# Kernel tuning notes

Hardware: AMD Instinct MI355X
Metric: run time of the kernel (lower is better)

Reference implementation:

```python
import jax, jax.numpy as jnp
import numpy as np

B, IN_LEN, NN, IN_DIM = 32, 28, 2048, 1
E, ND = 256, 256          # embed_dim, node_dim
H = E + ND                # hidden_dim = 512
N_LAYERS = 3
OUT_LEN = 28


def setup_inputs() -> dict:
    key = jax.random.key(0)
    ks = jax.random.split(key, 16)
    x_node = jax.random.normal(ks[0], (B, IN_LEN, NN, IN_DIM), jnp.float32)
    # x_state channels: [0]=cumulative cases, [1]=infected I, [2]=population N
    col0 = jax.random.uniform(ks[1], (B, IN_LEN, NN, 1), jnp.float32) * 100.0
    colI = jax.random.uniform(ks[2], (B, IN_LEN, NN, 1), jnp.float32) * 100.0 + 1.0
    colN = 1e4 * (1.0 + 0.1 * jax.random.uniform(ks[3], (B, IN_LEN, NN, 1), jnp.float32))
    x_state = jnp.concatenate([col0, colI, colN], axis=-1)
    node_emb = jax.random.normal(ks[4], (NN, ND), jnp.float32) * 0.05
    W_ts = jax.random.normal(ks[5], (E, IN_DIM * IN_LEN), jnp.float32) * 0.05
    b_ts = jnp.zeros((E,), jnp.float32)
    enc_W1 = jax.random.normal(ks[6], (N_LAYERS, H, H), jnp.float32) * 0.02
    enc_b1 = jnp.zeros((N_LAYERS, H), jnp.float32)
    enc_W2 = jax.random.normal(ks[7], (N_LAYERS, H, H), jnp.float32) * 0.02
    enc_b2 = jnp.zeros((N_LAYERS, H), jnp.float32)
    Wb = jax.random.normal(ks[8], (1, H), jnp.float32) * 0.05
    bb = jnp.zeros((1,), jnp.float32)
    Wg = jax.random.normal(ks[9], (1, H), jnp.float32) * 0.05
    bg = jnp.zeros((1,), jnp.float32)
    return dict(x_node=x_node, x_state=x_state, node_emb=node_emb,
                W_ts=W_ts, b_ts=b_ts, enc_W1=enc_W1, enc_b1=enc_b1,
                enc_W2=enc_W2, enc_b2=enc_b2, Wb=Wb, bb=bb, Wg=Wg, bg=bg)


def _forward(x_node, x_state, node_emb, W_ts, b_ts,
             enc_W1, enc_b1, enc_W2, enc_b2, Wb, bb, Wg, bg):
    Bn, Lh, Nn, _ = x_node.shape
    # [B,L,N,D] -> [B,N,L*D] (channel = in_dim*in_len for 1x1 conv == linear)
    flat = jnp.transpose(x_node[..., :IN_DIM], (0, 2, 1, 3)).reshape(Bn, Nn, Lh * IN_DIM)
    ts = flat @ W_ts.T + b_ts                                  # [B,N,E]
    h = jnp.concatenate(
        [ts, jnp.broadcast_to(node_emb[None], (Bn,) + node_emb.shape)], axis=-1)  # [B,N,H]
    for l in range(enc_W1.shape[0]):                            # residual MLP encoder
        z = jnp.maximum(h @ enc_W1[l].T + enc_b1[l], 0.0)
        h = h + z @ enc_W2[l].T + enc_b2[l]
    b = jax.nn.sigmoid(h @ Wb.T + bb)                           # [B,N,1] infection rate
    g = jax.nn.sigmoid(h @ Wg.T + bg)                           # [B,N,1] recovery rate

    Npop = x_state[:, -1, :, 2:3]                               # [B,N,1]
    I_hist = x_state[..., 1:2] / g[:, None]                     # [B,L,N,1]
    Iin_hist = jnp.maximum(
        I_hist[:, 1:] - I_hist[:, :-1] + x_state[:, :-1, :, 1:2], 0.0)  # [B,L-1,N,1]
    t1 = jnp.arange(Lh - 1, 0, -1, dtype=jnp.float32)
    w1 = jnp.exp(-g[:, None] * t1[None, :, None, None])         # [B,L-1,N,1]
    I_Tm1 = jnp.sum(w1 * Iin_hist, axis=1)                      # [B,N,1]
    R_Tm1 = Npop - x_state[:, -2, :, 0:1]
    S_Tm1 = Npop - I_Tm1 - R_Tm1
    Iin0 = b * S_Tm1 * I_Tm1 / Npop
    Rin0 = g * I_hist[:, -1, :, 0:1]
    Iin_hist = jnp.concatenate([Iin_hist, Iin0[:, None]], axis=1)  # [B,L,N,1]
    S = S_Tm1 - Iin0
    t2 = jnp.arange(Lh, 0, -1, dtype=jnp.float32)
    w2 = jnp.exp(-g[:, None] * t2[None, :, None, None])
    I = jnp.sum(w2 * Iin_hist, axis=1)                          # [B,N,1]
    R = R_Tm1 + Rin0

    # The torch loop recomputes sum_i exp(-g*(L-i))*Iin_i each step; exact identity:
    # I_new = exp(-g) * (I_old + Iin_new). O(T) scan instead of O(T^2).
    decay = jnp.exp(-g)

    def step(carry, _):
        S, I, R = carry
        Iin = b * S * I / Npop
        S = S - Iin
        Rin = g * I            # uses pre-update I_T, matching torch order
        I = decay * (I + Iin)
        R = R + Rin
        return (S, I, R), Rin

    _, rins = jax.lax.scan(step, (S, I, R), None, length=OUT_LEN)  # [T,B,N,1]
    return jnp.transpose(rins, (1, 0, 2, 3))                       # [B,out_len,N,1]


def reference(x_node, x_state, node_emb, W_ts, b_ts, enc_W1, enc_b1,
              enc_W2, enc_b2, Wb, bb, Wg, bg):
    return _forward(x_node, x_state, node_emb, W_ts, b_ts,
                    enc_W1, enc_b1, enc_W2, enc_b2, Wb, bb, Wg, bg)
```

## Files before the change

### kernel.cpp

```cpp
#include <hip/hip_runtime.h>
#include <hip/hip_bf16.h>
#include <math.h>

#define BATCH 32
#define IN_LEN 28
#define NN 2048
#define E 256
#define H 512
#define N_LAYERS 3
#define OUT_LEN 28
#define M_ROWS (BATCH * NN)

typedef unsigned short u16;
typedef unsigned int   u32;
typedef __attribute__((ext_vector_type(8))) short short8;
typedef __attribute__((ext_vector_type(4))) float f32x4;

#define WAITV(N)  asm volatile("s_waitcnt vmcnt(" #N ")" ::: "memory")
#define BARRIER() __builtin_amdgcn_s_barrier()

__device__ __forceinline__ u16 f2h(float x) {
    union { _Float16 h; u16 u; } v; v.h = (_Float16)x; return v.u;
}
__device__ __forceinline__ float h2f(u16 u) {
    union { _Float16 h; u16 u; } v; v.u = u; return (float)v.h;
}

__device__ __forceinline__ void gload_lds16(const void* g, void* l) {
    __builtin_amdgcn_global_load_lds(
        (const __attribute__((address_space(1))) void*)g,
        (__attribute__((address_space(3))) void*)l, 16, 0, 0);
}

__global__ __launch_bounds__(256)
void k_split2(const float* __restrict__ w1, const float* __restrict__ w2,
              u16* __restrict__ hi, u16* __restrict__ lo, int nW)
{
    int i = blockIdx.x * 256 + threadIdx.x;
    float v = (i < nW) ? w1[i] : w2[i - nW];
    u16 h = f2h(v);
    hi[i] = h;
    lo[i] = f2h(v - h2f(h));
}

__global__ __launch_bounds__(256)
void k_ts(const float* __restrict__ x_node, const float* __restrict__ node_emb,
          const float* __restrict__ W_ts, const float* __restrict__ b_ts,
          u16* __restrict__ hhi, u16* __restrict__ hlo)
{
    __shared__ float xs[IN_LEN][64];
    const int tid = threadIdx.x;
    const int b   = blockIdx.y;
    const int n0  = blockIdx.x * 64;
    const int c   = tid & 127;
    const int sec = tid >> 7;

    for (int idx = tid; idx < IN_LEN * 64; idx += 256) {
        int l = idx >> 6, i = idx & 63;
        xs[l][i] = x_node[((size_t)b * IN_LEN + l) * NN + n0 + i];
    }

    float w0[IN_LEN], w1[IN_LEN];
    float bias0 = 0.f, bias1 = 0.f;
    if (sec == 0) {
        #pragma unroll
        for (int j = 0; j < IN_LEN; j++) {
            w0[j] = W_ts[(2 * c) * IN_LEN + j];
            w1[j] = W_ts[(2 * c + 1) * IN_LEN + j];
        }
        bias0 = b_ts[2 * c];
        bias1 = b_ts[2 * c + 1];
    }
    __syncthreads();

    for (int i = 0; i < 64; i++) {
        size_t row = (size_t)b * NN + n0 + i;
        u32* oh = (u32*)(hhi + row * H);
        u32* ol = (u32*)(hlo + row * H);
        float v0, v1;
        int oc;
        if (sec == 0) {
            v0 = bias0; v1 = bias1;
            #pragma unroll
            for (int j = 0; j < IN_LEN; j++) {
                float x = xs[j][i];
                v0 += x * w0[j];
                v1 += x * w1[j];
            }
            oc = c;
        } else {
            const float2 ev = *(const float2*)&node_emb[(size_t)(n0 + i) * 256 + 2 * c];
            v0 = ev.x; v1 = ev.y;
            oc = 128 + c;
        }
        u16 h0 = f2h(v0), h1 = f2h(v1);
        oh[oc] = (u32)h0 | ((u32)h1 << 16);
        ol[oc] = (u32)f2h(v0 - h2f(h0)) | ((u32)f2h(v1 - h2f(h1)) << 16);
    }
}

__global__ __launch_bounds__(256)
void k_gemm1(const u16* __restrict__ Ahi, const u16* __restrict__ Alo,
             const u16* __restrict__ Whi, const u16* __restrict__ Wlo,
             const float* __restrict__ bias, u16* __restrict__ Z)
{
    __shared__ __align__(16) u16 smem[40960];

    const int tid = threadIdx.x;
    const int ln  = tid & 63;
    const int wv  = tid >> 6;

    const int id   = blockIdx.x;
    const int c    = (id >> 3) & 3;
    const int r    = (id & 7) | ((id >> 5) << 3);
    const int row0 = r * 128;
    const int col0 = c * 128;

    const int rbase = (wv & 1) * 64;
    const int cbase = (wv >> 1) * 64;

    const int lr = ln >> 2;
    const int lc = ln & 3;

    const u16* sgsrc; int sofs; int tb;
    if      (wv == 0) { sgsrc = Ahi; sofs = 0;     tb = row0; }
    else if (wv == 1) { sgsrc = Alo; sofs = 12288; tb = row0; }
    else if (wv == 2) { sgsrc = Whi; sofs = 24576; tb = col0; }
    else              { sgsrc = Wlo; sofs = 32768; tb = col0; }

    auto stage = [&](int p, int kt) {
        u16* dstbuf = smem + sofs + p * 4096;
        #pragma unroll
        for (int i = 0; i < 8; i++) {
            int row = i * 16 + lr;
            int sc  = lc ^ ((row >> 1) & 3);
            gload_lds16(sgsrc + (size_t)(tb + row) * H + kt + sc * 8,
                        dstbuf + i * 512);
        }
    };

    f32x4 acc[4][4];
    #pragma unroll
    for (int m = 0; m < 4; m++)
        #pragma unroll
        for (int n = 0; n < 4; n++) acc[m][n] = (f32x4)(0.f);

    stage(0, 0);
    if (wv < 2) stage(1, 32);

    const int wl = ln & 15;

    for (int t = 0; t < 16; t++) {
        if (wv < 2) { if (t < 15) { WAITV(8); } else { WAITV(0); } }
        else        { WAITV(0); }
        BARRIER();
        if (wv < 2) { if (t + 2 < 16) stage((t + 2) % 3, (t + 2) * 32); }
        else        { if (t + 1 < 16) stage((t + 1) & 1, (t + 1) * 32); }

        const int pa = t % 3, pw = t & 1;
        const u16* bAh = smem + 0     + pa * 4096;
        const u16* bAl = smem + 12288 + pa * 4096;
        const u16* bWh = smem + 24576 + pw * 4096;
        const u16* bWl = smem + 32768 + pw * 4096;

        short8 ahi[4], alo[4], whi[4], wlo[4];
        #pragma unroll
        for (int m = 0; m < 4; m++) {
            int rr = rbase + m * 16 + wl;
            int cc = ((ln >> 4) ^ ((rr >> 1) & 3)) * 8;
            ahi[m] = *(const short8*)&bAh[rr * 32 + cc];
            alo[m] = *(const short8*)&bAl[rr * 32 + cc];
        }
        #pragma unroll
        for (int n = 0; n < 4; n++) {
            int wr = cbase + n * 16 + wl;
            int cc = ((ln >> 4) ^ ((wr >> 1) & 3)) * 8;
            whi[n] = *(const short8*)&bWh[wr * 32 + cc];
            wlo[n] = *(const short8*)&bWl[wr * 32 + cc];
        }
        #pragma unroll
        for (int m = 0; m < 4; m++)
            #pragma unroll
            for (int n = 0; n < 4; n++) {
                acc[m][n] = __builtin_amdgcn_mfma_f32_16x16x32_f16(ahi[m], whi[n], acc[m][n], 0, 0, 0);
                acc[m][n] = __builtin_amdgcn_mfma_f32_16x16x32_f16(ahi[m], wlo[n], acc[m][n], 0, 0, 0);
                acc[m][n] = __builtin_amdgcn_mfma_f32_16x16x32_f16(alo[m], whi[n], acc[m][n], 0, 0, 0);
            }
    }

    __syncthreads();
    u16* zb = smem + wv * 4096;
    float bv[4];
    #pragma unroll
    for (int n = 0; n < 4; n++) bv[n] = bias[col0 + cbase + n * 16 + wl];
    #pragma unroll
    for (int m = 0; m < 4; m++)
        #pragma unroll
        for (int n = 0; n < 4; n++)
            #pragma unroll
            for (int rg = 0; rg < 4; rg++) {
                int row_l = m * 16 + (ln >> 4) * 4 + rg;
                zb[row_l * 64 + n * 16 + wl] =
                    f2h(fmaxf(acc[m][n][rg] + bv[n], 0.f));
            }
    const int cr = ln >> 3;
    const int cc = (ln & 7) * 8;
    #pragma unroll
    for (int p2 = 0; p2 < 8; p2++) {
        int row_l = cr + p2 * 8;
        uint4 v = *(const uint4*)&zb[row_l * 64 + cc];
        *(uint4*)&Z[(size_t)(row0 + rbase + row_l) * H + col0 + cbase + cc] = v;
    }
}

template <int HEAD>
__global__ __launch_bounds__(256)
void k_gemm2(const u16* __restrict__ Z,
             const u16* __restrict__ Whi, const u16* __restrict__ Wlo,
             const float* __restrict__ bias,
             u16* HHi, u16* HLo,
             const float* __restrict__ Wb, const float* __restrict__ Wg,
             float* __restrict__ bSum, float* __restrict__ gSum)
{
    __shared__ __align__(16) u16 smem[40960];

    const int tid = threadIdx.x;
    const int ln  = tid & 63;
    const int wv  = tid >> 6;

    const int id   = blockIdx.x;
    const int c    = (id >> 3) & 3;
    const int r    = (id & 7) | ((id >> 5) << 3);
    const int row0 = r * 128;
    const int col0 = c * 128;

    const int rbase = (wv & 1) * 64;
    const int cbase = (wv >> 1) * 64;

    const int lr = ln >> 2;
    const int lc = ln & 3;

    const u16* sgsrc; int sofs; int tb; int iofs; int niss;
    const bool zw = (wv == 0) || (wv == 3);
    if      (wv == 0) { sgsrc = Z;   sofs = 0;     tb = row0;      iofs = 0;    niss = 4; }
    else if (wv == 3) { sgsrc = Z;   sofs = 0;     tb = row0 + 64; iofs = 2048; niss = 4; }
    else if (wv == 1) { sgsrc = Whi; sofs = 16384; tb = col0;      iofs = 0;    niss = 8; }
    else              { sgsrc = Wlo; sofs = 28672; tb = col0;      iofs = 0;    niss = 8; }

    auto stage = [&](int p, int kt) {
        u16* dstbuf = smem + sofs + p * 4096 + iofs;
        #pragma unroll
        for (int i = 0; i < 8; i++) {
            if (i >= niss) break;
            int row = i * 16 + lr;
            int sc  = lc ^ ((row >> 1) & 3);
            gload_lds16(sgsrc + (size_t)(tb + row) * H + kt + sc * 8,
                        dstbuf + i * 512);
        }
    };

    f32x4 acc[4][4];
    #pragma unroll
    for (int m = 0; m < 4; m++)
        #pragma unroll
        for (int n = 0; n < 4; n++) acc[m][n] = (f32x4)(0.f);

    stage(0, 0);
    if (zw) { stage(1, 32); stage(2, 64); }
    else    { stage(1, 32); }

    const int wl = ln & 15;

    for (int t = 0; t < 16; t++) {
        if (zw) {
            if      (t < 14) { WAITV(8); }
            else if (t == 14){ WAITV(4); }
            else             { WAITV(0); }
        } else {
            if (t < 15) { WAITV(8); } else { WAITV(0); }
        }
        BARRIER();
        if (zw) { if (t + 3 < 16) stage((t + 3) & 3, (t + 3) * 32); }
        else    { if (t + 2 < 16) stage((t + 2) % 3, (t + 2) * 32); }

        const int pz = t & 3, pw = t % 3;
        const u16* bZ  = smem + 0     + pz * 4096;
        const u16* bWh = smem + 16384 + pw * 4096;
        const u16* bWl = smem + 28672 + pw * 4096;

        short8 az[4], whi[4], wlo[4];
        #pragma unroll
        for (int m = 0; m < 4; m++) {
            int rr = rbase + m * 16 + wl;
            int cc = ((ln >> 4) ^ ((rr >> 1) & 3)) * 8;
            az[m] = *(const short8*)&bZ[rr * 32 + cc];
        }
        #pragma unroll
        for (int n = 0; n < 4; n++) {
            int wr = cbase + n * 16 + wl;
            int cc = ((ln >> 4) ^ ((wr >> 1) & 3)) * 8;
            whi[n] = *(const short8*)&bWh[wr * 32 + cc];
            wlo[n] = *(const short8*)&bWl[wr * 32 + cc];
        }
        #pragma unroll
        for (int m = 0; m < 4; m++)
            #pragma unroll
            for (int n = 0; n < 4; n++) {
                acc[m][n] = __builtin_amdgcn_mfma_f32_16x16x32_f16(az[m], whi[n], acc[m][n], 0, 0, 0);
                acc[m][n] = __builtin_amdgcn_mfma_f32_16x16x32_f16(az[m], wlo[n], acc[m][n], 0, 0, 0);
            }
    }

    const int cr  = ln >> 3;
    const int ccl = (ln & 7) * 4;

    uint2  uhv[2][8], ulv[2][8];
    float4 bvv[2], hbv[2], hgv[2];
    #pragma unroll
    for (int nh = 0; nh < 2; nh++) {
        const int gc0 = col0 + cbase + nh * 32 + ccl;
        bvv[nh] = *(const float4*)&bias[gc0];
        if (HEAD) {
            hbv[nh] = *(const float4*)&Wb[gc0];
            hgv[nh] = *(const float4*)&Wg[gc0];
        }
        #pragma unroll
        for (int p2 = 0; p2 < 8; p2++) {
            size_t gidx = (size_t)(row0 + rbase + cr + p2 * 8) * H + gc0;
            uhv[nh][p2] = *(const uint2*)(HHi + gidx);
            ulv[nh][p2] = *(const uint2*)(HLo + gidx);
        }
    }

    BARRIER();
    float* fb = (float*)smem + wv * 2048;

    float pb[8], pg[8];
    if (HEAD) {
        #pragma unroll
        for (int p2 = 0; p2 < 8; p2++) { pb[p2] = 0.f; pg[p2] = 0.f; }
    }

    #pragma unroll
    for (int nh = 0; nh < 2; nh++) {
        #pragma unroll
        for (int m = 0; m < 4; m++)
            #pragma unroll
            for (int j = 0; j < 2; j++)
                #pragma unroll
                for (int rg = 0; rg < 4; rg++) {
                    int row_l = m * 16 + (ln >> 4) * 4 + rg;
                    fb[row_l * 32 + j * 16 + wl] = acc[m][nh * 2 + j][rg];
                }
        const int gc0 = col0 + cbase + nh * 32 + ccl;
        const float4 bv = bvv[nh];
        #pragma unroll
        for (int p2 = 0; p2 < 8; p2++) {
            int row_l = cr + p2 * 8;
            size_t gidx = (size_t)(row0 + rbase + row_l) * H + gc0;
            uint2 uh = uhv[nh][p2];
            uint2 ul = ulv[nh][p2];
            float4 a = *(const float4*)&fb[row_l * 32 + ccl];
            float v0 = a.x + bv.x + h2f((u16)(uh.x & 0xFFFF)) + h2f((u16)(ul.x & 0xFFFF));
            float v1 = a.y + bv.y + h2f((u16)(uh.x >> 16))    + h2f((u16)(ul.x >> 16));
            float v2 = a.z + bv.z + h2f((u16)(uh.y & 0xFFFF)) + h2f((u16)(ul.y & 0xFFFF));
            float v3 = a.w + bv.w + h2f((u16)(uh.y >> 16))    + h2f((u16)(ul.y >> 16));
            if (HEAD) {
                pb[p2] += v0 * hbv[nh].x + v1 * hbv[nh].y + v2 * hbv[nh].z + v3 * hbv[nh].w;
                pg[p2] += v0 * hgv[nh].x + v1 * hgv[nh].y + v2 * hgv[nh].z + v3 * hgv[nh].w;
            } else {
                u16 h0 = f2h(v0), h1 = f2h(v1), h2 = f2h(v2), h3 = f2h(v3);
                uint2 oh, ol;
                oh.x = (u32)h0 | ((u32)h1 << 16);
                oh.y = (u32)h2 | ((u32)h3 << 16);
                ol.x = (u32)f2h(v0 - h2f(h0)) | ((u32)f2h(v1 - h2f(h1)) << 16);
                ol.y = (u32)f2h(v2 - h2f(h2)) | ((u32)f2h(v3 - h2f(h3)) << 16);
                *(uint2*)(HHi + gidx) = oh;
                *(uint2*)(HLo + gidx) = ol;
            }
        }
    }

    if (HEAD) {
        #pragma unroll
        for (int p2 = 0; p2 < 8; p2++) {
            float sb = pb[p2], sg = pg[p2];
            #pragma unroll
            for (int off = 1; off < 8; off <<= 1) {
                sb += __shfl_xor(sb, off);
                sg += __shfl_xor(sg, off);
            }
            if ((ln & 7) == 0) {
                int grow = row0 + rbase + cr + p2 * 8;
                atomicAdd(&bSum[grow], sb);
                atomicAdd(&gSum[grow], sg);
            }
        }
    }
}

__global__ __launch_bounds__(256)
void k_sir(const float* __restrict__ x_state,
           const float* __restrict__ bSum, const float* __restrict__ gSum,
           const float* __restrict__ bb, const float* __restrict__ bg,
           float* __restrict__ out)
{
    const int row = blockIdx.x * 256 + threadIdx.x;
    const int bb_ = row / NN;
    const int n   = row % NN;

    const float g = 1.f / (1.f + expf(-(gSum[row] + bg[0])));
    const float b = 1.f / (1.f + expf(-(bSum[row] + bb[0])));
    const float d = expf(-g);

    const float* xs = x_state + ((size_t)bb_ * IN_LEN) * (NN * 3) + (size_t)n * 3;

    float x1_prev = xs[1];
    float Ih_prev = x1_prev / g;
    float acc = 0.f;
    #pragma unroll 4
    for (int t = 1; t <= IN_LEN - 1; ++t) {
        float x1 = xs[(size_t)t * (NN * 3) + 1];
        float Ih = x1 / g;
        float Iin = fmaxf(Ih - Ih_prev + x1_prev, 0.f);
        acc = acc * d + Iin;
        Ih_prev = Ih;
        x1_prev = x1;
    }
    float ITm1 = acc * d;
    float Npop = xs[(size_t)(IN_LEN - 1) * (NN * 3) + 2];
    float RTm1 = Npop - xs[(size_t)(IN_LEN - 2) * (NN * 3) + 0];
    float STm1 = Npop - ITm1 - RTm1;
    float Iin0 = b * STm1 * ITm1 / Npop;
    float S = STm1 - Iin0;
    float I = d * (ITm1 + Iin0);

    float* op = out + ((size_t)bb_ * OUT_LEN) * NN + n;
    #pragma unroll 4
    for (int k = 0; k < OUT_LEN; k++) {
        float Iin = b * S * I / Npop;
        S = S - Iin;
        float Rin = g * I;
        I = d * (I + Iin);
        op[(size_t)k * NN] = Rin;
    }
}

extern "C" void kernel_launch(void* const* d_in, const int* in_sizes, int n_in,
                              void* d_out, int out_size, void* d_ws, size_t ws_size,
                              hipStream_t stream)
{
    const float* x_node   = (const float*)d_in[0];
    const float* x_state  = (const float*)d_in[1];
    const float* node_emb = (const float*)d_in[2];
    const float* W_ts     = (const float*)d_in[3];
    const float* b_ts     = (const float*)d_in[4];
    const float* enc_W1   = (const float*)d_in[5];
    const float* enc_b1   = (const float*)d_in[6];
    const float* enc_W2   = (const float*)d_in[7];
    const float* enc_b2   = (const float*)d_in[8];
    const float* Wb       = (const float*)d_in[9];
    const float* bb       = (const float*)d_in[10];
    const float* Wg       = (const float*)d_in[11];
    const float* bg       = (const float*)d_in[12];
    float* out = (float*)d_out;

    u16* hhi   = (u16*)d_ws;
    u16* hlo   = hhi + (size_t)M_ROWS * H;
    u16* wHi   = hlo + (size_t)M_ROWS * H;
    u16* wLo   = wHi + (size_t)6 * H * H;
    float* bSum = (float*)(wLo + (size_t)6 * H * H);
    float* gSum = bSum + M_ROWS;
    u16* z     = (u16*)(gSum + M_ROWS);

    size_t used  = (size_t)((char*)z - (char*)d_ws);
    size_t avail = (ws_size > used) ? ws_size - used : 0;
    long long chunkLL = (long long)(avail / (H * sizeof(u16))) & ~1023LL;
    int chunk = (chunkLL > M_ROWS) ? M_ROWS : (int)chunkLL;
    if (chunk < 1024) chunk = 1024;

    hipMemsetAsync(bSum, 0, 2 * (size_t)M_ROWS * sizeof(float), stream);

    const int nW = N_LAYERS * H * H;
    k_split2<<<2 * nW / 256, 256, 0, stream>>>(enc_W1, enc_W2, wHi, wLo, nW);

    k_ts<<<dim3(NN / 64, BATCH), 256, 0, stream>>>(x_node, node_emb, W_ts, b_ts, hhi, hlo);

    for (int l = 0; l < N_LAYERS; l++) {
        const u16* W1hi = wHi + (size_t)l * H * H;
        const u16* W1lo = wLo + (size_t)l * H * H;
        const u16* W2hi = wHi + (size_t)nW + (size_t)l * H * H;
        const u16* W2lo = wLo + (size_t)nW + (size_t)l * H * H;
        const float* b1 = enc_b1 + (size_t)l * H;
        const float* b2 = enc_b2 + (size_t)l * H;
        for (int r = 0; r < M_ROWS; r += chunk) {
            int rows = (M_ROWS - r < chunk) ? (M_ROWS - r) : chunk;
            u16* hrhi = hhi + (size_t)r * H;
            u16* hrlo = hlo + (size_t)r * H;
            int nblk = (rows / 128) * 4;
            k_gemm1<<<nblk, 256, 0, stream>>>(hrhi, hrlo, W1hi, W1lo, b1, z);
            if (l < N_LAYERS - 1)
                k_gemm2<0><<<nblk, 256, 0, stream>>>(z, W2hi, W2lo, b2, hrhi, hrlo,
                                                     Wb, Wg, bSum + r, gSum + r);
            else
                k_gemm2<1><<<nblk, 256, 0, stream>>>(z, W2hi, W2lo, b2, hrhi, hrlo,
                                                     Wb, Wg, bSum + r, gSum + r);
        }
    }

    k_sir<<<M_ROWS / 256, 256, 0, stream>>>(x_state, bSum, gSum, bb, bg, out);
}
```

Measured before the change: 726.2 us.

## Enlarge gemm1 tiles to 256x256 with 512-thread blocks and interleaved staging

Result: no change. 724.4 us (-0.2%).

```diff
diff --git a/kernel.cpp b/kernel.cpp
--- a/kernel.cpp
+++ b/kernel.cpp
@@ -17,6 +17,8 @@
 typedef __attribute__((ext_vector_type(4))) float f32x4;
 
 #define WAITV(N)  asm volatile("s_waitcnt vmcnt(" #N ")" ::: "memory")
+#define WAITLGKM0() do { asm volatile("s_waitcnt lgkmcnt(0)" ::: "memory"); \
+                         __builtin_amdgcn_sched_barrier(0); } while (0)
 #define BARRIER() __builtin_amdgcn_s_barrier()
 
 __device__ __forceinline__ u16 f2h(float x) {
@@ -99,102 +101,113 @@
     }
 }
 
-__global__ __launch_bounds__(256)
+__global__ __launch_bounds__(512, 2)
 void k_gemm1(const u16* __restrict__ Ahi, const u16* __restrict__ Alo,
              const u16* __restrict__ Whi, const u16* __restrict__ Wlo,
              const float* __restrict__ bias, u16* __restrict__ Z)
 {
-    __shared__ __align__(16) u16 smem[40960];
+    __shared__ __align__(16) u16 smem[65536];
 
     const int tid = threadIdx.x;
     const int ln  = tid & 63;
     const int wv  = tid >> 6;
 
     const int id   = blockIdx.x;
-    const int c    = (id >> 3) & 3;
-    const int r    = (id & 7) | ((id >> 5) << 3);
-    const int row0 = r * 128;
-    const int col0 = c * 128;
-
-    const int rbase = (wv & 1) * 64;
-    const int cbase = (wv >> 1) * 64;
+    const int r    = id >> 1;
+    const int c    = id & 1;
+    const int row0 = r * 256;
+    const int col0 = c * 256;
+
+    const int wr = wv >> 2;
+    const int wc = wv & 3;
+
+    const int strm = wv >> 1;
+    const int q    = wv & 1;
+    const u16* sgsrc = (strm == 0) ? Ahi : (strm == 1) ? Alo
+                     : (strm == 2) ? Whi : Wlo;
+    const int sofs = strm * 16384;
+    const int tb   = (strm < 2) ? row0 : col0;
 
     const int lr = ln >> 2;
     const int lc = ln & 3;
 
-    const u16* sgsrc; int sofs; int tb;
-    if      (wv == 0) { sgsrc = Ahi; sofs = 0;     tb = row0; }
-    else if (wv == 1) { sgsrc = Alo; sofs = 12288; tb = row0; }
-    else if (wv == 2) { sgsrc = Whi; sofs = 24576; tb = col0; }
-    else              { sgsrc = Wlo; sofs = 32768; tb = col0; }
-
-    auto stage = [&](int p, int kt) {
-        u16* dstbuf = smem + sofs + p * 4096;
-        #pragma unroll
-        for (int i = 0; i < 8; i++) {
-            int row = i * 16 + lr;
-            int sc  = lc ^ ((row >> 1) & 3);
-            gload_lds16(sgsrc + (size_t)(tb + row) * H + kt + sc * 8,
-                        dstbuf + i * 512);
-        }
+    auto stage1 = [&](int p, int i, int kt) {
+        u16* dstbuf = smem + sofs + p * 8192 + q * 4096;
+        int row = i * 16 + lr;
+        int sc  = lc ^ ((row >> 1) & 3);
+        gload_lds16(sgsrc + (size_t)(tb + q * 128 + row) * H + kt + sc * 8,
+                    dstbuf + i * 512);
     };
 
-    f32x4 acc[4][4];
-    #pragma unroll
-    for (int m = 0; m < 4; m++)
+    f32x4 acc[8][4];
+    #pragma unroll
+    for (int m = 0; m < 8; m++)
         #pragma unroll
         for (int n = 0; n < 4; n++) acc[m][n] = (f32x4)(0.f);
 
-    stage(0, 0);
-    if (wv < 2) stage(1, 32);
+    #pragma unroll
+    for (int i = 0; i < 8; i++) stage1(0, i, 0);
 
     const int wl = ln & 15;
 
+    #pragma unroll 1
     for (int t = 0; t < 16; t++) {
-        if (wv < 2) { if (t < 15) { WAITV(8); } else { WAITV(0); } }
-        else        { WAITV(0); }
-        BARRIER();
-        if (wv < 2) { if (t + 2 < 16) stage((t + 2) % 3, (t + 2) * 32); }
-        else        { if (t + 1 < 16) stage((t + 1) & 1, (t + 1) * 32); }
-
-        const int pa = t % 3, pw = t & 1;
-        const u16* bAh = smem + 0     + pa * 4096;
-        const u16* bAl = smem + 12288 + pa * 4096;
-        const u16* bWh = smem + 24576 + pw * 4096;
-        const u16* bWl = smem + 32768 + pw * 4096;
-
-        short8 ahi[4], alo[4], whi[4], wlo[4];
-        #pragma unroll
-        for (int m = 0; m < 4; m++) {
-            int rr = rbase + m * 16 + wl;
-            int cc = ((ln >> 4) ^ ((rr >> 1) & 3)) * 8;
-            ahi[m] = *(const short8*)&bAh[rr * 32 + cc];
-            alo[m] = *(const short8*)&bAl[rr * 32 + cc];
-        }
-        #pragma unroll
-        for (int n = 0; n < 4; n++) {
-            int wr = cbase + n * 16 + wl;
-            int cc = ((ln >> 4) ^ ((wr >> 1) & 3)) * 8;
-            whi[n] = *(const short8*)&bWh[wr * 32 + cc];
-            wlo[n] = *(const short8*)&bWl[wr * 32 + cc];
-        }
-        #pragma unroll
-        for (int m = 0; m < 4; m++)
-            #pragma unroll
-            for (int n = 0; n < 4; n++) {
-                acc[m][n] = __builtin_amdgcn_mfma_f32_16x16x32_f16(ahi[m], whi[n], acc[m][n], 0, 0, 0);
-                acc[m][n] = __builtin_amdgcn_mfma_f32_16x16x32_f16(ahi[m], wlo[n], acc[m][n], 0, 0, 0);
-                acc[m][n] = __builtin_amdgcn_mfma_f32_16x16x32_f16(alo[m], whi[n], acc[m][n], 0, 0, 0);
-            }
+        __syncthreads();
+
+        const int pb = t & 1;
+        const u16* bAh = smem + 0     + pb * 8192;
+        const u16* bAl = smem + 16384 + pb * 8192;
+        const u16* bWh = smem + 32768 + pb * 8192;
+        const u16* bWl = smem + 49152 + pb * 8192;
+
+        short8 whi[4], wlo[4];
+
+        #pragma unroll
+        for (int p = 0; p < 4; p++) {
+            short8 ah[2], al[2];
+            #pragma unroll
+            for (int m2 = 0; m2 < 2; m2++) {
+                int rr = wr * 128 + (p * 2 + m2) * 16 + wl;
+                int cc = ((ln >> 4) ^ ((rr >> 1) & 3)) * 8;
+                ah[m2] = *(const short8*)&bAh[rr * 32 + cc];
+                al[m2] = *(const short8*)&bAl[rr * 32 + cc];
+            }
+            if (p == 0) {
+                #pragma unroll
+                for (int n = 0; n < 4; n++) {
+                    int wrr = wc * 64 + n * 16 + wl;
+                    int cc = ((ln >> 4) ^ ((wrr >> 1) & 3)) * 8;
+                    whi[n] = *(const short8*)&bWh[wrr * 32 + cc];
+                    wlo[n] = *(const short8*)&bWl[wrr * 32 + cc];
+                }
+            }
+            if (p < 2 && t + 1 < 16) {
+                #pragma unroll
+                for (int j = 0; j < 4; j++)
+                    stage1(1 - pb, p * 4 + j, (t + 1) * 32);
+            }
+            WAITLGKM0();
+            __builtin_amdgcn_s_setprio(1);
+            #pragma unroll
+            for (int m2 = 0; m2 < 2; m2++)
+                #pragma unroll
+                for (int n = 0; n < 4; n++) {
+                    acc[p*2+m2][n] = __builtin_amdgcn_mfma_f32_16x16x32_f16(ah[m2], whi[n], acc[p*2+m2][n], 0, 0, 0);
+                    acc[p*2+m2][n] = __builtin_amdgcn_mfma_f32_16x16x32_f16(ah[m2], wlo[n], acc[p*2+m2][n], 0, 0, 0);
+                    acc[p*2+m2][n] = __builtin_amdgcn_mfma_f32_16x16x32_f16(al[m2], whi[n], acc[p*2+m2][n], 0, 0, 0);
+                }
+            __builtin_amdgcn_s_setprio(0);
+            if (p < 3) BARRIER();
+        }
     }
 
     __syncthreads();
-    u16* zb = smem + wv * 4096;
+    u16* zb = smem + wv * 8192;
     float bv[4];
     #pragma unroll
-    for (int n = 0; n < 4; n++) bv[n] = bias[col0 + cbase + n * 16 + wl];
-    #pragma unroll
-    for (int m = 0; m < 4; m++)
+    for (int n = 0; n < 4; n++) bv[n] = bias[col0 + wc * 64 + n * 16 + wl];
+    #pragma unroll
+    for (int m = 0; m < 8; m++)
         #pragma unroll
         for (int n = 0; n < 4; n++)
             #pragma unroll
@@ -203,13 +216,13 @@
                 zb[row_l * 64 + n * 16 + wl] =
                     f2h(fmaxf(acc[m][n][rg] + bv[n], 0.f));
             }
-    const int cr = ln >> 3;
-    const int cc = (ln & 7) * 8;
-    #pragma unroll
-    for (int p2 = 0; p2 < 8; p2++) {
+    const int cr  = ln >> 3;
+    const int ccx = (ln & 7) * 8;
+    #pragma unroll
+    for (int p2 = 0; p2 < 16; p2++) {
         int row_l = cr + p2 * 8;
-        uint4 v = *(const uint4*)&zb[row_l * 64 + cc];
-        *(uint4*)&Z[(size_t)(row0 + rbase + row_l) * H + col0 + cbase + cc] = v;
+        uint4 v = *(const uint4*)&zb[row_l * 64 + ccx];
+        *(uint4*)&Z[(size_t)(row0 + wr * 128 + row_l) * H + col0 + wc * 64 + ccx] = v;
     }
 }
 
@@ -497,8 +510,8 @@
             int rows = (M_ROWS - r < chunk) ? (M_ROWS - r) : chunk;
             u16* hrhi = hhi + (size_t)r * H;
             u16* hrlo = hlo + (size_t)r * H;
+            k_gemm1<<<(rows / 256) * 2, 512, 0, stream>>>(hrhi, hrlo, W1hi, W1lo, b1, z);
             int nblk = (rows / 128) * 4;
-            k_gemm1<<<nblk, 256, 0, stream>>>(hrhi, hrlo, W1hi, W1lo, b1, z);
             if (l < N_LAYERS - 1)
                 k_gemm2<0><<<nblk, 256, 0, stream>>>(z, W2hi, W2lo, b2, hrhi, hrlo,
                                                      Wb, Wg, bSum + r, gSum + r);
```
